# Optimization experiments

Hardware: AMD Instinct MI355X
Metric: run time of the kernel (lower is better)

The kernel has to match this reference:

```python
import jax, jax.numpy as jnp
import numpy as np

N_NODES = 40000      # batch of group nodes
DEGREE = 32          # neighbors (members) per node
NUM_USERS = 100000
NUM_GROUPS = 50000
EMBED_DIM = 64


def setup_inputs() -> dict:
    key = jax.random.key(0)
    ks = jax.random.split(key, 8)
    E = N_NODES * DEGREE
    d = EMBED_DIM
    return {
        "nodes": jax.random.randint(ks[0], (N_NODES,), 0, NUM_GROUPS),
        "neigh_idx": jax.random.randint(ks[1], (E,), 0, NUM_USERS),
        # edge i belongs to node segment_ids[i]; sorted, DEGREE edges per node
        "segment_ids": jnp.repeat(jnp.arange(N_NODES), DEGREE),
        "u2e_weight": jax.random.normal(ks[2], (NUM_USERS, d), jnp.float32) * 0.02,
        "g2e_weight": jax.random.normal(ks[3], (NUM_GROUPS, d), jnp.float32) * 0.02,
        "att1_w": jax.random.normal(ks[4], (d, 2 * d), jnp.float32) * (1.0 / np.sqrt(2 * d)),
        "att1_b": jnp.zeros((d,), jnp.float32),
        "att2_w": jax.random.normal(ks[5], (d, d), jnp.float32) * (1.0 / np.sqrt(d)),
        "att2_b": jnp.zeros((d,), jnp.float32),
        "att3_w": jax.random.normal(ks[6], (1, d), jnp.float32) * (1.0 / np.sqrt(d)),
        "att3_b": jnp.zeros((1,), jnp.float32),
    }


def _segment_softmax(logits, seg, num_segments):
    # numerically stable softmax within each node's neighbor segment
    m = jax.ops.segment_max(logits, seg, num_segments=num_segments)
    a = jnp.exp(logits - m[seg])
    s = jax.ops.segment_sum(a, seg, num_segments=num_segments)
    return a / s[seg]


def reference(nodes, neigh_idx, segment_ids, u2e_weight, g2e_weight,
              att1_w, att1_b, att2_w, att2_b, att3_w, att3_b):
    e_u = u2e_weight[neigh_idx]                 # [E, d] member embeddings
    g_rep = g2e_weight[nodes][segment_ids]      # [E, d] group query broadcast per edge
    x = jnp.concatenate([e_u, g_rep], axis=-1)  # [E, 2d]
    h = jax.nn.relu(x @ att1_w.T + att1_b)      # [E, d] (dropout inactive at eval)
    h = jax.nn.relu(h @ att2_w.T + att2_b)      # [E, d]
    logits = (h @ att3_w.T + att3_b)[:, 0]      # [E]
    att = _segment_softmax(logits, segment_ids, N_NODES)  # [E]
    # attention-weighted aggregation of member embeddings per node
    return jax.ops.segment_sum(att[:, None] * e_u, segment_ids, num_segments=N_NODES)  # [N, d]
```

## Files before the change

### kernel.cpp

```cpp
#include <hip/hip_runtime.h>
#include <hip/hip_bf16.h>

typedef __attribute__((ext_vector_type(8))) short short8;
typedef __attribute__((ext_vector_type(4))) float floatx4;
typedef __attribute__((ext_vector_type(2))) float float2v;
typedef __attribute__((ext_vector_type(4))) unsigned int uintx4;

#define NNODES 40000
#define NPW 4
#define WAVES 8
#define NPB (NPW * WAVES)
#define NBLK (NNODES / NPB)

#define U2E_ELEMS (100000 * 64)
#define WS_ALIGN 256
#define WS_NEEDED ((size_t)U2E_ELEMS * 2 + WS_ALIGN)


__device__ __forceinline__ float bf2f(unsigned short s) {
    return __uint_as_float(((unsigned int)s) << 16);
}
__device__ __forceinline__ unsigned short f2bf(float f) {
    unsigned int u = __float_as_uint(f);
    u += 0x7fffu + ((u >> 16) & 1u);
    return (unsigned short)(u >> 16);
}
__device__ __forceinline__ unsigned int pk2bf(float lo, float hi) {
#if __has_builtin(__builtin_amdgcn_cvt_pk_bf16_f32)
    auto r = __builtin_amdgcn_cvt_pk_bf16_f32(lo, hi);
    unsigned int u; __builtin_memcpy(&u, &r, 4);
    return u;
#else
    return (unsigned int)f2bf(lo) | ((unsigned int)f2bf(hi) << 16);
#endif
}
__device__ __forceinline__ short8 cvt8(const float* fp) {
    floatx4 a = *(const floatx4*)fp;
    floatx4 b = *(const floatx4*)(fp + 4);
    uintx4 u;
    u[0] = pk2bf(a[0], a[1]); u[1] = pk2bf(a[2], a[3]);
    u[2] = pk2bf(b[0], b[1]); u[3] = pk2bf(b[2], b[3]);
    short8 r; __builtin_memcpy(&r, &u, 16);
    return r;
}
__device__ __forceinline__ short8 u4s8(uintx4 u) {
    short8 r; __builtin_memcpy(&r, &u, 16);
    return r;
}

__device__ __forceinline__ float2v f2pair(floatx4 v, int i) {
    return (float2v){v[2 * i], v[2 * i + 1]};
}
__device__ __forceinline__ float2v fma2(float2v a, float2v b, float2v c) {
#if __has_builtin(__builtin_elementwise_fma)
    return __builtin_elementwise_fma(a, b, c);
#else
    return (float2v){fmaf(a[0], b[0], c[0]), fmaf(a[1], b[1], c[1])};
#endif
}
__device__ __forceinline__ float2v relu2(float2v a) {
#if __has_builtin(__builtin_elementwise_max)
    return __builtin_elementwise_max(a, (float2v)(0.f));
#else
    return (float2v){fmaxf(a[0], 0.f), fmaxf(a[1], 0.f)};
#endif
}

template<int CTRL>
__device__ __forceinline__ float dppadd(float v) {
#if __has_builtin(__builtin_amdgcn_update_dpp)
    int y = __builtin_amdgcn_update_dpp(0, __float_as_int(v), CTRL, 0xf, 0xf, true);
    return v + __int_as_float(y);
#else
    return v + __shfl_xor(v, (CTRL == 0xB1) ? 1 : (CTRL == 0x4E) ? 2 : (CTRL == 0x141) ? 4 : 8, 64);
#endif
}
__device__ __forceinline__ float swz16add(float v) {
#if __has_builtin(__builtin_amdgcn_ds_swizzle)
    int y = __builtin_amdgcn_ds_swizzle(__float_as_int(v), 0x401F);
    return v + __int_as_float(y);
#else
    return v + __shfl_xor(v, 16, 64);
#endif
}

__global__ __launch_bounds__(256) void convert_u2e(
    const float* __restrict__ u2e, unsigned short* __restrict__ ub) {
    const size_t i = ((size_t)blockIdx.x * 256 + threadIdx.x) * 8;
    if (i < U2E_ELEMS) *(short8*)(ub + i) = cvt8(u2e + i);
}

__device__ __forceinline__ int sigma_row(int dt, int m) {
    return (dt & 1) * 32 + (m >> 2) * 8 + ((dt >> 1) << 2) + (m & 3);
}

template<int PRE>
__global__ __launch_bounds__(512, 4) void gat_fused(
    const int*   __restrict__ nodes,
    const int*   __restrict__ neigh,
    const float* __restrict__ u2f,
    const unsigned short* __restrict__ u2b,
    const float* __restrict__ g2e,
    const float* __restrict__ w1,
    const float* __restrict__ b1,
    const float* __restrict__ w2,
    const float* __restrict__ b2,
    const float* __restrict__ w3,
    float* __restrict__ out)
{
    __shared__ alignas(16) short w1f[16 * 64 * 8];
    __shared__ alignas(16) short w2f[8 * 64 * 8];
    __shared__ alignas(16) short ebuf[WAVES][2048];
    __shared__ alignas(16) float abuf[WAVES][64];
    __shared__ alignas(16) float bvec[192];

    const int tid  = threadIdx.x;
    const int wv   = tid >> 6;
    const int lane = tid & 63;
    const int q    = lane >> 4;
    const int n16  = lane & 15;

    for (int i = tid; i < 16 * 64; i += 512) {
        int s = i >> 6, slot = i & 63;
        int dt = s >> 2, kc = s & 3;
        int row = sigma_row(dt, slot & 15);
        int k   = kc * 32 + (slot >> 4) * 8;
        *(short8*)&w1f[i * 8] = cvt8(w1 + (size_t)row * 128 + k);
    }
    for (int i = tid; i < 8 * 64; i += 512) {
        int s = i >> 6, slot = i & 63;
        int ot = s >> 1, kc = s & 1;
        int row = sigma_row(ot, slot & 15);
        int k   = kc * 32 + (slot >> 4) * 8;
        *(short8*)&w2f[i * 8] = cvt8(w2 + (size_t)row * 64 + k);
    }
    for (int i = tid; i < 192; i += 512)
        bvec[i] = (i < 64) ? b1[i] : (i < 128) ? b2[i - 64] : w3[i - 128];
    __syncthreads();

    const int n0 = blockIdx.x * NPB + wv * NPW;

    const int ew0 = n16 * 64 + ((q ^ (n16 & 7)) * 8);
    const int ew1 = n16 * 64 + (((4 + q) ^ (n16 & 7)) * 8);

    const int hh = lane >> 5;
    const int mm = lane & 31;
    int bofs[8];
    #pragma unroll
    for (int p = 0; p < 8; ++p)
        bofs[p] = hh * 1024 + ((((mm >> 2) ^ p) << 3) + ((mm & 3) << 1));
    const int dimo = (mm << 1) | hh;

    int gn, d0, d1;
    short8 A00, A01, A10, A11, G0, G1;

    auto loadA = [&](int idx, int half) -> short8 {
        if (PRE) return *(const short8*)(u2b + (size_t)idx * 64 + half * 32 + q * 8);
        else     return cvt8(u2f + (size_t)idx * 64 + half * 32 + q * 8);
    };

    {
        int g0i = nodes[n0];
        size_t eb0 = (size_t)n0 * 32;
        int c0 = neigh[eb0 + n16];
        int c1 = neigh[eb0 + 16 + n16];
        A00 = loadA(c0, 0); A01 = loadA(c0, 1);
        A10 = loadA(c1, 0); A11 = loadA(c1, 1);
        G0  = cvt8(g2e + (size_t)g0i * 64 + q * 8);
        G1  = cvt8(g2e + (size_t)g0i * 64 + 32 + q * 8);
        int n1 = n0 + 1;
        gn = nodes[n1];
        size_t eb1 = (size_t)n1 * 32;
        d0 = neigh[eb1 + n16];
        d1 = neigh[eb1 + 16 + n16];
    }

    const floatx4 zero4 = {0.f, 0.f, 0.f, 0.f};
    int qo = q * 8;

    for (int it = 0; it < NPW; ++it) {
        const int n = n0 + it;
        const short8 a00 = A00, a01 = A01, a10 = A10, a11 = A11, g0 = G0, g1 = G1;

        floatx4 acc1[2][4];
        #pragma unroll
        for (int et = 0; et < 2; ++et)
            #pragma unroll
            for (int dt = 0; dt < 4; ++dt) acc1[et][dt] = zero4;
        #pragma unroll
        for (int kc = 0; kc < 4; ++kc) {
            const short8 x0 = (kc == 0) ? a00 : (kc == 1) ? a01 : (kc == 2) ? g0 : g1;
            const short8 x1 = (kc == 0) ? a10 : (kc == 1) ? a11 : (kc == 2) ? g0 : g1;
            #pragma unroll
            for (int dt = 0; dt < 4; ++dt) {
                const short8 w = *(const short8*)&w1f[((dt * 4 + kc) * 64 + lane) * 8];
                acc1[0][dt] = __builtin_amdgcn_mfma_f32_16x16x32_bf16(w, x0, acc1[0][dt], 0, 0, 0);
                acc1[1][dt] = __builtin_amdgcn_mfma_f32_16x16x32_bf16(w, x1, acc1[1][dt], 0, 0, 0);
            }
        }

        {
            short* ebw = &ebuf[wv][0];
            *(short8*)&ebw[ew0]        = a00;
            *(short8*)&ebw[ew1]        = a01;
            *(short8*)&ebw[ew0 + 1024] = a10;
            *(short8*)&ebw[ew1 + 1024] = a11;
        }

        if (it < NPW - 1) {
            A00 = loadA(d0, 0); A01 = loadA(d0, 1);
            A10 = loadA(d1, 0); A11 = loadA(d1, 1);
            G0  = cvt8(g2e + (size_t)gn * 64 + qo);
            G1  = cvt8(g2e + (size_t)gn * 64 + 32 + qo);
            int nn = n0 + it + 2; if (nn > NNODES - 1) nn = NNODES - 1;
            gn = nodes[nn];
            size_t eb2 = (size_t)nn * 32;
            d0 = neigh[eb2 + n16];
            d1 = neigh[eb2 + 16 + n16];
        }

        asm volatile("" : "+v"(qo));

        floatx4 B1[2][2];
        B1[0][0] = *(const floatx4*)&bvec[qo];
        B1[0][1] = *(const floatx4*)&bvec[qo + 4];
        B1[1][0] = *(const floatx4*)&bvec[qo + 32];
        B1[1][1] = *(const floatx4*)&bvec[qo + 36];
        short8 y[2][2];
        #pragma unroll
        for (int kc2 = 0; kc2 < 2; ++kc2)
            #pragma unroll
            for (int et = 0; et < 2; ++et) {
                float2v p0 = relu2(f2pair(acc1[et][kc2], 0)     + f2pair(B1[kc2][0], 0));
                float2v p1 = relu2(f2pair(acc1[et][kc2], 1)     + f2pair(B1[kc2][0], 1));
                float2v p2 = relu2(f2pair(acc1[et][kc2 + 2], 0) + f2pair(B1[kc2][1], 0));
                float2v p3 = relu2(f2pair(acc1[et][kc2 + 2], 1) + f2pair(B1[kc2][1], 1));
                uintx4 u;
                u[0] = pk2bf(p0[0], p0[1]);
                u[1] = pk2bf(p1[0], p1[1]);
                u[2] = pk2bf(p2[0], p2[1]);
                u[3] = pk2bf(p3[0], p3[1]);
                y[kc2][et] = u4s8(u);
            }

        floatx4 acc2[2][4];
        #pragma unroll
        for (int et = 0; et < 2; ++et)
            #pragma unroll
            for (int ot = 0; ot < 4; ++ot) acc2[et][ot] = zero4;
        #pragma unroll
        for (int kc2 = 0; kc2 < 2; ++kc2)
            #pragma unroll
            for (int ot = 0; ot < 4; ++ot) {
                const short8 w = *(const short8*)&w2f[((ot * 2 + kc2) * 64 + lane) * 8];
                acc2[0][ot] = __builtin_amdgcn_mfma_f32_16x16x32_bf16(w, y[kc2][0], acc2[0][ot], 0, 0, 0);
                acc2[1][ot] = __builtin_amdgcn_mfma_f32_16x16x32_bf16(w, y[kc2][1], acc2[1][ot], 0, 0, 0);
            }

        floatx4 B2[2][2], W3[2][2];
        B2[0][0] = *(const floatx4*)&bvec[qo + 64];
        B2[0][1] = *(const floatx4*)&bvec[qo + 68];
        B2[1][0] = *(const floatx4*)&bvec[qo + 96];
        B2[1][1] = *(const floatx4*)&bvec[qo + 100];
        W3[0][0] = *(const floatx4*)&bvec[qo + 128];
        W3[0][1] = *(const floatx4*)&bvec[qo + 132];
        W3[1][0] = *(const floatx4*)&bvec[qo + 160];
        W3[1][1] = *(const floatx4*)&bvec[qo + 164];
        float2v s0v = (float2v)(0.f), s1v = (float2v)(0.f);
        #pragma unroll
        for (int ot = 0; ot < 4; ++ot) {
            const int h = ot & 1, g = ot >> 1;
            const float2v b2a = f2pair(B2[h][g], 0), b2b = f2pair(B2[h][g], 1);
            const float2v w3a = f2pair(W3[h][g], 0), w3b = f2pair(W3[h][g], 1);
            s0v = fma2(relu2(f2pair(acc2[0][ot], 0) + b2a), w3a, s0v);
            s0v = fma2(relu2(f2pair(acc2[0][ot], 1) + b2b), w3b, s0v);
            s1v = fma2(relu2(f2pair(acc2[1][ot], 0) + b2a), w3a, s1v);
            s1v = fma2(relu2(f2pair(acc2[1][ot], 1) + b2b), w3b, s1v);
        }
        float s0 = s0v[0] + s0v[1];
        float s1 = s1v[0] + s1v[1];
        s0 += __shfl_xor(s0, 16, 64); s0 += __shfl_xor(s0, 32, 64);
        s1 += __shfl_xor(s1, 16, 64); s1 += __shfl_xor(s1, 32, 64);
        const float lg = ((lane >> 4) & 1) ? s1 : s0;

        const short* ebw = &ebuf[wv][0];
        unsigned int eu[16];
        #pragma unroll
        for (int k = 0; k < 16; ++k)
            eu[k] = *(const unsigned int*)&ebw[bofs[k & 7] + k * 64];

        const float ex = __expf(lg);
        float sm = dppadd<0xB1>(ex);
        sm = dppadd<0x4E>(sm);
        sm = dppadd<0x141>(sm);
        sm = dppadd<0x140>(sm);
        sm = swz16add(sm);
#if __has_builtin(__builtin_amdgcn_rcpf)
        const float attv = ex * __builtin_amdgcn_rcpf(sm);
#else
        const float attv = ex / sm;
#endif

        *(float2v*)&abuf[wv][mm * 2] = (float2v){attv, attv};
        {
            const float* abp = &abuf[wv][hh * 32];
            float2v ac0 = (float2v)(0.f), ac1 = (float2v)(0.f);
            #pragma unroll
            for (int k = 0; k < 16; k += 2) {
                const float2v ap0 = *(const float2v*)&abp[2 * k];
                const float2v ap1 = *(const float2v*)&abp[2 * k + 2];
                const unsigned int u0 = eu[k];
                const unsigned int u1 = eu[k + 1];
                float2v e0, e1;
                e0[0] = __uint_as_float(u0 << 16);
                e0[1] = __uint_as_float(u0 & 0xffff0000u);
                e1[0] = __uint_as_float(u1 << 16);
                e1[1] = __uint_as_float(u1 & 0xffff0000u);
                ac0 = fma2(ap0, e0, ac0);
                ac1 = fma2(ap1, e1, ac1);
            }
            const float2v acp = ac0 + ac1;
            const float lt = acp[0] + __shfl_xor(acp[0], 32, 64);
            const float ht = acp[1] + __shfl_xor(acp[1], 32, 64);
            out[(size_t)n * 64 + dimo] = hh ? ht : lt;
        }
    }
}

extern "C" void kernel_launch(void* const* d_in, const int* in_sizes, int n_in,
                              void* d_out, int out_size, void* d_ws, size_t ws_size,
                              hipStream_t stream) {
    const int*   nodes = (const int*)d_in[0];
    const int*   neigh = (const int*)d_in[1];
    const float* u2e = (const float*)d_in[3];
    const float* g2e = (const float*)d_in[4];
    const float* w1  = (const float*)d_in[5];
    const float* b1  = (const float*)d_in[6];
    const float* w2  = (const float*)d_in[7];
    const float* b2  = (const float*)d_in[8];
    const float* w3  = (const float*)d_in[9];
    float* out = (float*)d_out;

    if (ws_size >= WS_NEEDED) {
        unsigned short* ub = (unsigned short*)(((uintptr_t)d_ws + WS_ALIGN - 1) & ~(uintptr_t)(WS_ALIGN - 1));
        hipLaunchKernelGGL(convert_u2e, dim3((U2E_ELEMS / 8 + 255) / 256), dim3(256),
                           0, stream, u2e, ub);
        hipLaunchKernelGGL(gat_fused<1>, dim3(NBLK), dim3(512), 0, stream,
                           nodes, neigh, u2e, ub, g2e, w1, b1, w2, b2, w3, out);
    } else {
        hipLaunchKernelGGL(gat_fused<0>, dim3(NBLK), dim3(512), 0, stream,
                           nodes, neigh, u2e, (const unsigned short*)nullptr,
                           g2e, w1, b1, w2, b2, w3, out);
    }
}
```

Before: 157.1 us.

## Precompute group-query half of first attention layer once per node

The group-embedding contribution to the first MLP layer is the same for all 32 edges of a node. It is now computed once per node in a block prologue by two waves using MFMA, stored in shared memory, and added as a per-node bias. This removes half of the layer-1 MFMAs and the per-node g2e loads from the main loop. The cost is an extra barrier, a serial prologue on two waves, and more shared memory (about 8.7KB), which may affect occupancy.

```diff
diff --git a/kernel.cpp b/kernel.cpp
--- a/kernel.cpp
+++ b/kernel.cpp
@@ -113,6 +113,7 @@
     __shared__ alignas(16) short ebuf[WAVES][2048];
     __shared__ alignas(16) float abuf[WAVES][64];
     __shared__ alignas(16) float bvec[192];
+    __shared__ alignas(16) float gb1f[32 * 68];
 
     const int tid  = threadIdx.x;
     const int wv   = tid >> 6;
@@ -136,6 +137,22 @@
     }
     for (int i = tid; i < 192; i += 512)
         bvec[i] = (i < 64) ? b1[i] : (i < 128) ? b2[i - 64] : w3[i - 128];
+    __syncthreads();
+
+    if (wv < 2) {
+        const int gnode = nodes[blockIdx.x * NPB + wv * 16 + n16];
+        const short8 gf0 = cvt8(g2e + (size_t)gnode * 64 + q * 8);
+        const short8 gf1 = cvt8(g2e + (size_t)gnode * 64 + 32 + q * 8);
+        #pragma unroll
+        for (int dt = 0; dt < 4; ++dt) {
+            floatx4 ga = {0.f, 0.f, 0.f, 0.f};
+            const short8 wA = *(const short8*)&w1f[((dt * 4 + 2) * 64 + lane) * 8];
+            const short8 wB = *(const short8*)&w1f[((dt * 4 + 3) * 64 + lane) * 8];
+            ga = __builtin_amdgcn_mfma_f32_16x16x32_bf16(wA, gf0, ga, 0, 0, 0);
+            ga = __builtin_amdgcn_mfma_f32_16x16x32_bf16(wB, gf1, ga, 0, 0, 0);
+            *(floatx4*)&gb1f[(wv * 16 + n16) * 68 + (dt & 1) * 32 + q * 8 + (dt >> 1) * 4] = ga;
+        }
+    }
     __syncthreads();
 
     const int n0 = blockIdx.x * NPB + wv * NPW;
@@ -151,8 +168,8 @@
         bofs[p] = hh * 1024 + ((((mm >> 2) ^ p) << 3) + ((mm & 3) << 1));
     const int dimo = (mm << 1) | hh;
 
-    int gn, d0, d1;
-    short8 A00, A01, A10, A11, G0, G1;
+    int d0, d1;
+    short8 A00, A01, A10, A11;
 
     auto loadA = [&](int idx, int half) -> short8 {
         if (PRE) return *(const short8*)(u2b + (size_t)idx * 64 + half * 32 + q * 8);
@@ -160,17 +177,12 @@
     };
 
     {
-        int g0i = nodes[n0];
         size_t eb0 = (size_t)n0 * 32;
         int c0 = neigh[eb0 + n16];
         int c1 = neigh[eb0 + 16 + n16];
         A00 = loadA(c0, 0); A01 = loadA(c0, 1);
         A10 = loadA(c1, 0); A11 = loadA(c1, 1);
-        G0  = cvt8(g2e + (size_t)g0i * 64 + q * 8);
-        G1  = cvt8(g2e + (size_t)g0i * 64 + 32 + q * 8);
-        int n1 = n0 + 1;
-        gn = nodes[n1];
-        size_t eb1 = (size_t)n1 * 32;
+        size_t eb1 = (size_t)(n0 + 1) * 32;
         d0 = neigh[eb1 + n16];
         d1 = neigh[eb1 + 16 + n16];
     }
@@ -180,7 +192,7 @@
 
     for (int it = 0; it < NPW; ++it) {
         const int n = n0 + it;
-        const short8 a00 = A00, a01 = A01, a10 = A10, a11 = A11, g0 = G0, g1 = G1;
+        const short8 a00 = A00, a01 = A01, a10 = A10, a11 = A11;
 
         floatx4 acc1[2][4];
         #pragma unroll
@@ -188,9 +200,9 @@
             #pragma unroll
             for (int dt = 0; dt < 4; ++dt) acc1[et][dt] = zero4;
         #pragma unroll
-        for (int kc = 0; kc < 4; ++kc) {
-            const short8 x0 = (kc == 0) ? a00 : (kc == 1) ? a01 : (kc == 2) ? g0 : g1;
-            const short8 x1 = (kc == 0) ? a10 : (kc == 1) ? a11 : (kc == 2) ? g0 : g1;
+        for (int kc = 0; kc < 2; ++kc) {
+            const short8 x0 = (kc == 0) ? a00 : a01;
+            const short8 x1 = (kc == 0) ? a10 : a11;
             #pragma unroll
             for (int dt = 0; dt < 4; ++dt) {
                 const short8 w = *(const short8*)&w1f[((dt * 4 + kc) * 64 + lane) * 8];
@@ -210,10 +222,7 @@
         if (it < NPW - 1) {
             A00 = loadA(d0, 0); A01 = loadA(d0, 1);
             A10 = loadA(d1, 0); A11 = loadA(d1, 1);
-            G0  = cvt8(g2e + (size_t)gn * 64 + qo);
-            G1  = cvt8(g2e + (size_t)gn * 64 + 32 + qo);
             int nn = n0 + it + 2; if (nn > NNODES - 1) nn = NNODES - 1;
-            gn = nodes[nn];
             size_t eb2 = (size_t)nn * 32;
             d0 = neigh[eb2 + n16];
             d1 = neigh[eb2 + 16 + n16];
@@ -221,11 +230,12 @@
 
         asm volatile("" : "+v"(qo));
 
+        const float* gbp = &gb1f[(wv * NPW + it) * 68];
         floatx4 B1[2][2];
-        B1[0][0] = *(const floatx4*)&bvec[qo];
-        B1[0][1] = *(const floatx4*)&bvec[qo + 4];
-        B1[1][0] = *(const floatx4*)&bvec[qo + 32];
-        B1[1][1] = *(const floatx4*)&bvec[qo + 36];
+        B1[0][0] = *(const floatx4*)&bvec[qo]      + *(const floatx4*)&gbp[qo];
+        B1[0][1] = *(const floatx4*)&bvec[qo + 4]  + *(const floatx4*)&gbp[qo + 4];
+        B1[1][0] = *(const floatx4*)&bvec[qo + 32] + *(const floatx4*)&gbp[qo + 32];
+        B1[1][1] = *(const floatx4*)&bvec[qo + 36] + *(const floatx4*)&gbp[qo + 36];
         short8 y[2][2];
         #pragma unroll
         for (int kc2 = 0; kc2 < 2; ++kc2)
```

Result: faster. 150.7 us (-4.1%).
